# Kernel tuning notes

Hardware: AMD Instinct MI355X
Metric: run time of the kernel (lower is better)

## Reference

```python
import jax, jax.numpy as jnp
import numpy as np

THRESHOLD = 1.0   # spiking threshold (also used for reset detection)
BETA = 0.95       # reservoir membrane decay
N = 2048          # reservoir_size


def _heaviside(x):
    # snntorch Heaviside: (x > 0).float()
    return (x > 0).astype(x.dtype)


def setup_inputs() -> dict:
    key = jax.random.key(0)
    k1, k2, k3 = jax.random.split(key, 3)
    B, T = 32, 500
    x = jax.random.normal(k1, (B, T, 1), dtype=jnp.float32)
    # recurrent connectivity matrix loaded from .npy in the original; random here
    W = jax.random.normal(k2, (N, N), dtype=jnp.float32) / jnp.sqrt(jnp.float32(N))
    # nn.Linear default bias init: U(-1/sqrt(N), 1/sqrt(N))
    bound = 1.0 / np.sqrt(N)
    b = jax.random.uniform(k3, (N,), dtype=jnp.float32, minval=-bound, maxval=bound)
    return {"x": x, "W": W, "b": b}


def reference(x, W, b):
    """RLeaky reservoir with reset_mechanism='zero', reset_delay=True.
    Per step (snntorch RLeaky semantics):
      reset   = heaviside(mem_prev - threshold)            (detached)
      base    = beta*mem_prev + input + W @ spk_prev + b
      mem_new = base - reset*base                          ('zero' reset)
      spk_new = heaviside(mem_new - threshold)
    Input current = scalar x_t broadcast across all N neurons.
    """
    B = x.shape[0]
    Wt = W.T  # (N, N), spk @ W.T == Linear(spk)

    def step(carry, x_t):
        spk, mem = carry  # each (B, N)
        reset = _heaviside(mem - THRESHOLD)
        base = BETA * mem + x_t + spk @ Wt + b  # x_t: (B,1) broadcasts over N
        mem_new = base * (1.0 - reset)
        spk_new = _heaviside(mem_new - THRESHOLD)
        return (spk_new, mem_new), (spk_new, mem_new)

    init = (jnp.zeros((B, N), x.dtype), jnp.zeros((B, N), x.dtype))
    xs = jnp.swapaxes(x, 0, 1)  # (T, B, 1)
    _, (spk_rec, mem_rec) = jax.lax.scan(step, init, xs)
    avg_firing_rate = spk_rec.mean()
    return avg_firing_rate, spk_rec, mem_rec
```

## Files before the change

### kernel.cpp

```cpp
#include <hip/hip_runtime.h>

#define NN 2048
#define NB 32
#define NT 500
#define WGS 1024
#define NWG 256


__global__ void init_kernel(const float* __restrict__ x,
                            unsigned int* __restrict__ bitsG,
                            float* __restrict__ mem_ws,
                            float* __restrict__ xT,
                            int* __restrict__ wgcnt) {
    int g = blockIdx.x * blockDim.x + threadIdx.x;
    if (g < 2 * NN) bitsG[g] = 0u;
    if (g < NN * NB) mem_ws[g] = 0.0f;
    if (g < NT * NB) xT[g] = x[(size_t)(g & 31) * NT + (g >> 5)];
    if (g < NWG) wgcnt[g] = 0;
}

__launch_bounds__(WGS, 4)
__global__ void step_kernel(const float* __restrict__ W,
                            const float* __restrict__ bias,
                            float* __restrict__ out,
                            unsigned int* __restrict__ bitsG,
                            float* __restrict__ mem_ws,
                            const float* __restrict__ xT,
                            int* __restrict__ wgcnt,
                            int step)
{
    __shared__ unsigned int lbits[NN];
    __shared__ float lpart[8][8][32];
    __shared__ float lout[2][NB][9];
    __shared__ int   lcnt[4];

    const int wg = blockIdx.x;
    const int t  = threadIdx.x;
    const int i0 = wg * 8;
    const int cur = step & 1;

    ((uint2*)lbits)[t] = ((const uint2*)(bitsG + (size_t)cur * NN))[t];

    const int rh = t >> 8;
    const int jh = (t >> 5) & 7;
    const int b  = t & 31;

    float mem = 0.0f, xv = 0.0f, biasv = 0.0f;
    if (t < 256) {
        const int cil = t >> 5, cb = t & 31;
        mem   = mem_ws[(size_t)(i0 + cil) * NB + cb];
        xv    = xT[step * NB + cb];
        biasv = bias[i0 + cil];
    }

    const float4* __restrict__ wr0 = (const float4*)(W + (size_t)(i0 + 2 * rh    ) * NN) + jh * 64;
    const float4* __restrict__ wr1 = (const float4*)(W + (size_t)(i0 + 2 * rh + 1) * NN) + jh * 64;

    __syncthreads();

    float c0 = 0.0f, c1 = 0.0f;
    const uint4* bp = ((const uint4*)lbits) + jh * 64;
    #pragma unroll 4
    for (int jj = 0; jj < 64; ++jj) {
        const float4 w0 = wr0[jj];
        const float4 w1 = wr1[jj];
        const uint4  bu = bp[jj];
        float s;
        s = (float)((bu.x >> b) & 1u); c0 = fmaf(w0.x, s, c0); c1 = fmaf(w1.x, s, c1);
        s = (float)((bu.y >> b) & 1u); c0 = fmaf(w0.y, s, c0); c1 = fmaf(w1.y, s, c1);
        s = (float)((bu.z >> b) & 1u); c0 = fmaf(w0.z, s, c0); c1 = fmaf(w1.z, s, c1);
        s = (float)((bu.w >> b) & 1u); c0 = fmaf(w0.w, s, c0); c1 = fmaf(w1.w, s, c1);
    }
    lpart[jh][2 * rh    ][b] = c0;
    lpart[jh][2 * rh + 1][b] = c1;
    __syncthreads();

    if (t < 256) {
        const int cil = t >> 5;
        const int cb  = t & 31;

        float d = lpart[0][cil][cb];
        #pragma unroll
        for (int k = 1; k < 8; ++k) d += lpart[k][cil][cb];

        float sp = (float)((lbits[i0 + cil] >> cb) & 1u);

        float base = 0.95f * mem + xv + d + biasv;
        float nm   = base * (1.0f - sp);
        float ns   = (nm > 1.0f) ? 1.0f : 0.0f;

        mem_ws[(size_t)(i0 + cil) * NB + cb] = nm;

        unsigned long long bal = __ballot(ns > 0.5f);
        unsigned int* bw = bitsG + (size_t)(1 - cur) * NN;
        const int l  = t & 63;
        const int w2 = t >> 6;
        if (l == 0)  bw[i0 + 2 * w2]     = (unsigned int)(bal & 0xFFFFFFFFull);
        if (l == 32) bw[i0 + 2 * w2 + 1] = (unsigned int)(bal >> 32);
        if (l == 0)  lcnt[w2] = __popcll(bal);

        lout[0][cb][cil] = ns;
        lout[1][cb][cil] = nm;
    }
    __syncthreads();

    if (t == 0) wgcnt[wg] += lcnt[0] + lcnt[1] + lcnt[2] + lcnt[3];

    if (t < 512) {
        float* spk_rec = out + 1;
        float* mem_rec = out + 1 + (size_t)NT * NB * NN;
        const int arr = t >> 8;
        const int r2  = t & 255;
        const int bb  = r2 >> 3;
        const int il  = r2 & 7;
        size_t o = ((size_t)step * NB + bb) * (size_t)NN + i0 + il;
        if (arr == 0) __builtin_nontemporal_store(lout[0][bb][il], &spk_rec[o]);
        else          __builtin_nontemporal_store(lout[1][bb][il], &mem_rec[o]);
    }
}

__global__ void final_kernel(float* __restrict__ out, const int* __restrict__ wgcnt) {
    long long s = 0;
    for (int k = 0; k < NWG; ++k) s += wgcnt[k];
    out[0] = (float)((double)s / (double)((long long)NT * NB * NN));
}

extern "C" void kernel_launch(void* const* d_in, const int* in_sizes, int n_in,
                              void* d_out, int out_size, void* d_ws, size_t ws_size,
                              hipStream_t stream) {
    const float* x    = (const float*)d_in[0];
    const float* W    = (const float*)d_in[1];
    const float* bias = (const float*)d_in[2];
    float* out = (float*)d_out;

    unsigned int* bitsG  = (unsigned int*)d_ws;
    float*        mem_ws = (float*)((char*)d_ws + 16384);
    float*        xT     = (float*)((char*)d_ws + 278528);
    int*          wgcnt  = (int*)((char*)d_ws + 344064);

    init_kernel<<<dim3(256), dim3(256), 0, stream>>>(x, bitsG, mem_ws, xT, wgcnt);
    for (int step = 0; step < NT; ++step) {
        step_kernel<<<dim3(NWG), dim3(WGS), 0, stream>>>(W, bias, out, bitsG,
                                                         mem_ws, xT, wgcnt, step);
    }
    final_kernel<<<dim3(1), dim3(1), 0, stream>>>(out, wgcnt);
}
```

Baseline: 9.404 ms.

## Fuse time loop into persistent cooperative kernel with tagged spike-bit flags

Replaces the 500 per-step kernel launches with one cooperative persistent kernel that loops over all time steps. Membrane state stays in registers instead of global memory. Workgroups sync through per-word step tags packed into 64-bit spike-bit entries, polled with relaxed agent-scope atomics, rather than kernel boundaries. This removes launch overhead and the global round trip for membrane state, at the cost of relying on relaxed-ordering spin-polling across all 256 co-resident workgroups.

```diff
diff --git a/kernel.cpp b/kernel.cpp
--- a/kernel.cpp
+++ b/kernel.cpp
@@ -1,4 +1,7 @@
 #include <hip/hip_runtime.h>
+#include <hip/hip_cooperative_groups.h>
+
+namespace cg = cooperative_groups;
 
 #define NN 2048
 #define NB 32
@@ -7,122 +10,158 @@
 #define NWG 256
 
 
-__global__ void init_kernel(const float* __restrict__ x,
-                            unsigned int* __restrict__ bitsG,
-                            float* __restrict__ mem_ws,
-                            float* __restrict__ xT,
-                            int* __restrict__ wgcnt) {
-    int g = blockIdx.x * blockDim.x + threadIdx.x;
-    if (g < 2 * NN) bitsG[g] = 0u;
-    if (g < NN * NB) mem_ws[g] = 0.0f;
-    if (g < NT * NB) xT[g] = x[(size_t)(g & 31) * NT + (g >> 5)];
-    if (g < NWG) wgcnt[g] = 0;
-}
+__launch_bounds__(WGS, 4)
+__global__ void reservoir_kernel(const float* __restrict__ x,
+                                 const float* __restrict__ W,
+                                 const float* __restrict__ bias,
+                                 float* __restrict__ out,
+                                 void* __restrict__ wsv)
+{
+    cg::grid_group grid = cg::this_grid();
 
-__launch_bounds__(WGS, 4)
-__global__ void step_kernel(const float* __restrict__ W,
-                            const float* __restrict__ bias,
-                            float* __restrict__ out,
-                            unsigned int* __restrict__ bitsG,
-                            float* __restrict__ mem_ws,
-                            const float* __restrict__ xT,
-                            int* __restrict__ wgcnt,
-                            int step)
-{
     __shared__ unsigned int lbits[NN];
     __shared__ float lpart[8][8][32];
     __shared__ float lout[2][NB][9];
     __shared__ int   lcnt[4];
 
+    unsigned long long* bitsG2 = (unsigned long long*)wsv;
+    float* xT    = (float*)((char*)wsv + 32768);
+    int*   wgpart = (int*)((char*)wsv + 98304);
+
     const int wg = blockIdx.x;
     const int t  = threadIdx.x;
     const int i0 = wg * 8;
-    const int cur = step & 1;
 
-    ((uint2*)lbits)[t] = ((const uint2*)(bitsG + (size_t)cur * NN))[t];
+    if (t < 8) {
+        __hip_atomic_store(&bitsG2[i0 + t], 0ull,
+                           __ATOMIC_RELAXED, __HIP_MEMORY_SCOPE_AGENT);
+        __hip_atomic_store(&bitsG2[NN + i0 + t], 0xFFFFFFFF00000000ull,
+                           __ATOMIC_RELAXED, __HIP_MEMORY_SCOPE_AGENT);
+    }
+    for (int g = wg * WGS + t; g < NT * NB; g += NWG * WGS)
+        xT[g] = x[(size_t)(g & 31) * NT + (g >> 5)];
 
     const int rh = t >> 8;
     const int jh = (t >> 5) & 7;
     const int b  = t & 31;
 
-    float mem = 0.0f, xv = 0.0f, biasv = 0.0f;
-    if (t < 256) {
-        const int cil = t >> 5, cb = t & 31;
-        mem   = mem_ws[(size_t)(i0 + cil) * NB + cb];
-        xv    = xT[step * NB + cb];
-        biasv = bias[i0 + cil];
-    }
-
     const float4* __restrict__ wr0 = (const float4*)(W + (size_t)(i0 + 2 * rh    ) * NN) + jh * 64;
     const float4* __restrict__ wr1 = (const float4*)(W + (size_t)(i0 + 2 * rh + 1) * NN) + jh * 64;
 
+    const int cil = t >> 5;
+    const int cb  = t & 31;
+    const float biasv = (t < 256) ? bias[i0 + cil] : 0.0f;
+    float mem = 0.0f;
+    int   cnt = 0;
+
+    float* spk_rec = out + 1;
+    float* mem_rec = out + 1 + (size_t)NT * NB * NN;
+
+    grid.sync();
+
+    for (int step = 0; step < NT; ++step) {
+        const int cur = step & 1;
+        const unsigned int tag = (unsigned int)step;
+        const unsigned long long* src = bitsG2 + (size_t)cur * NN;
+
+        {
+            unsigned long long v;
+            for (;;) {
+                v = __hip_atomic_load(&src[t], __ATOMIC_RELAXED,
+                                      __HIP_MEMORY_SCOPE_AGENT);
+                if ((unsigned int)(v >> 32) == tag) break;
+                __builtin_amdgcn_s_sleep(1);
+            }
+            lbits[t] = (unsigned int)v;
+            for (;;) {
+                v = __hip_atomic_load(&src[t + 1024], __ATOMIC_RELAXED,
+                                      __HIP_MEMORY_SCOPE_AGENT);
+                if ((unsigned int)(v >> 32) == tag) break;
+                __builtin_amdgcn_s_sleep(1);
+            }
+            lbits[t + 1024] = (unsigned int)v;
+        }
+        const float xv = (t < 256) ? xT[step * NB + cb] : 0.0f;
+        __syncthreads();
+
+        float c0 = 0.0f, c1 = 0.0f;
+        const uint4* bp = ((const uint4*)lbits) + jh * 64;
+        #pragma unroll 4
+        for (int jj = 0; jj < 64; ++jj) {
+            const float4 w0 = wr0[jj];
+            const float4 w1 = wr1[jj];
+            const uint4  bu = bp[jj];
+            float s;
+            s = (float)((bu.x >> b) & 1u); c0 = fmaf(w0.x, s, c0); c1 = fmaf(w1.x, s, c1);
+            s = (float)((bu.y >> b) & 1u); c0 = fmaf(w0.y, s, c0); c1 = fmaf(w1.y, s, c1);
+            s = (float)((bu.z >> b) & 1u); c0 = fmaf(w0.z, s, c0); c1 = fmaf(w1.z, s, c1);
+            s = (float)((bu.w >> b) & 1u); c0 = fmaf(w0.w, s, c0); c1 = fmaf(w1.w, s, c1);
+        }
+        lpart[jh][2 * rh    ][b] = c0;
+        lpart[jh][2 * rh + 1][b] = c1;
+        __syncthreads();
+
+        if (t < 256) {
+            float d = lpart[0][cil][cb];
+            #pragma unroll
+            for (int k = 1; k < 8; ++k) d += lpart[k][cil][cb];
+
+            const float sp = (float)((lbits[i0 + cil] >> cb) & 1u);
+
+            float base = 0.95f * mem + xv + d + biasv;
+            float nm   = base * (1.0f - sp);
+            float ns   = (nm > 1.0f) ? 1.0f : 0.0f;
+            mem = nm;
+            cnt += (int)ns;
+
+            unsigned long long bal = __ballot(ns > 0.5f);
+            unsigned long long* dst = bitsG2 + (size_t)(1 - cur) * NN;
+            const unsigned long long tg = ((unsigned long long)(step + 1)) << 32;
+            const int l  = t & 63;
+            const int w2 = t >> 6;
+            if (l == 0)
+                __hip_atomic_store(&dst[i0 + 2 * w2],
+                                   tg | (unsigned int)(bal & 0xFFFFFFFFull),
+                                   __ATOMIC_RELAXED, __HIP_MEMORY_SCOPE_AGENT);
+            if (l == 32)
+                __hip_atomic_store(&dst[i0 + 2 * w2 + 1],
+                                   tg | (unsigned int)(bal >> 32),
+                                   __ATOMIC_RELAXED, __HIP_MEMORY_SCOPE_AGENT);
+            if (l == 0) lcnt[w2] = __popcll(bal);
+
+            lout[0][cb][cil] = ns;
+            lout[1][cb][cil] = nm;
+        }
+        __syncthreads();
+
+        if (t < 512) {
+            const int arr = t >> 8;
+            const int r2  = t & 255;
+            const int bb  = r2 >> 3;
+            const int il  = r2 & 7;
+            size_t o = ((size_t)step * NB + bb) * (size_t)NN + i0 + il;
+            if (arr == 0) __builtin_nontemporal_store(lout[0][bb][il], &spk_rec[o]);
+            else          __builtin_nontemporal_store(lout[1][bb][il], &mem_rec[o]);
+        }
+    }
+
+    #pragma unroll
+    for (int d2 = 1; d2 < 64; d2 <<= 1) cnt += __shfl_xor(cnt, d2, 64);
+    if ((t & 63) == 0 && t < 256) lcnt[t >> 6] = cnt;
     __syncthreads();
-
-    float c0 = 0.0f, c1 = 0.0f;
-    const uint4* bp = ((const uint4*)lbits) + jh * 64;
-    #pragma unroll 4
-    for (int jj = 0; jj < 64; ++jj) {
-        const float4 w0 = wr0[jj];
-        const float4 w1 = wr1[jj];
-        const uint4  bu = bp[jj];
-        float s;
-        s = (float)((bu.x >> b) & 1u); c0 = fmaf(w0.x, s, c0); c1 = fmaf(w1.x, s, c1);
-        s = (float)((bu.y >> b) & 1u); c0 = fmaf(w0.y, s, c0); c1 = fmaf(w1.y, s, c1);
-        s = (float)((bu.z >> b) & 1u); c0 = fmaf(w0.z, s, c0); c1 = fmaf(w1.z, s, c1);
-        s = (float)((bu.w >> b) & 1u); c0 = fmaf(w0.w, s, c0); c1 = fmaf(w1.w, s, c1);
+    if (t == 0) wgpart[wg] = lcnt[0] + lcnt[1] + lcnt[2] + lcnt[3];
+    grid.sync();
+    if (wg == 0) {
+        int ps = (t < NWG) ? wgpart[t] : 0;
+        #pragma unroll
+        for (int d2 = 1; d2 < 64; d2 <<= 1) ps += __shfl_xor(ps, d2, 64);
+        if ((t & 63) == 0 && t < 256) lcnt[t >> 6] = ps;
+        __syncthreads();
+        if (t == 0) {
+            long long s2 = (long long)lcnt[0] + lcnt[1] + lcnt[2] + lcnt[3];
+            out[0] = (float)((double)s2 / (double)((long long)NT * NB * NN));
+        }
     }
-    lpart[jh][2 * rh    ][b] = c0;
-    lpart[jh][2 * rh + 1][b] = c1;
-    __syncthreads();
-
-    if (t < 256) {
-        const int cil = t >> 5;
-        const int cb  = t & 31;
-
-        float d = lpart[0][cil][cb];
-        #pragma unroll
-        for (int k = 1; k < 8; ++k) d += lpart[k][cil][cb];
-
-        float sp = (float)((lbits[i0 + cil] >> cb) & 1u);
-
-        float base = 0.95f * mem + xv + d + biasv;
-        float nm   = base * (1.0f - sp);
-        float ns   = (nm > 1.0f) ? 1.0f : 0.0f;
-
-        mem_ws[(size_t)(i0 + cil) * NB + cb] = nm;
-
-        unsigned long long bal = __ballot(ns > 0.5f);
-        unsigned int* bw = bitsG + (size_t)(1 - cur) * NN;
-        const int l  = t & 63;
-        const int w2 = t >> 6;
-        if (l == 0)  bw[i0 + 2 * w2]     = (unsigned int)(bal & 0xFFFFFFFFull);
-        if (l == 32) bw[i0 + 2 * w2 + 1] = (unsigned int)(bal >> 32);
-        if (l == 0)  lcnt[w2] = __popcll(bal);
-
-        lout[0][cb][cil] = ns;
-        lout[1][cb][cil] = nm;
-    }
-    __syncthreads();
-
-    if (t == 0) wgcnt[wg] += lcnt[0] + lcnt[1] + lcnt[2] + lcnt[3];
-
-    if (t < 512) {
-        float* spk_rec = out + 1;
-        float* mem_rec = out + 1 + (size_t)NT * NB * NN;
-        const int arr = t >> 8;
-        const int r2  = t & 255;
-        const int bb  = r2 >> 3;
-        const int il  = r2 & 7;
-        size_t o = ((size_t)step * NB + bb) * (size_t)NN + i0 + il;
-        if (arr == 0) __builtin_nontemporal_store(lout[0][bb][il], &spk_rec[o]);
-        else          __builtin_nontemporal_store(lout[1][bb][il], &mem_rec[o]);
-    }
-}
-
-__global__ void final_kernel(float* __restrict__ out, const int* __restrict__ wgcnt) {
-    long long s = 0;
-    for (int k = 0; k < NWG; ++k) s += wgcnt[k];
-    out[0] = (float)((double)s / (double)((long long)NT * NB * NN));
 }
 
 extern "C" void kernel_launch(void* const* d_in, const int* in_sizes, int n_in,
@@ -132,16 +171,9 @@
     const float* W    = (const float*)d_in[1];
     const float* bias = (const float*)d_in[2];
     float* out = (float*)d_out;
+    void*  ws  = d_ws;
 
-    unsigned int* bitsG  = (unsigned int*)d_ws;
-    float*        mem_ws = (float*)((char*)d_ws + 16384);
-    float*        xT     = (float*)((char*)d_ws + 278528);
-    int*          wgcnt  = (int*)((char*)d_ws + 344064);
-
-    init_kernel<<<dim3(256), dim3(256), 0, stream>>>(x, bitsG, mem_ws, xT, wgcnt);
-    for (int step = 0; step < NT; ++step) {
-        step_kernel<<<dim3(NWG), dim3(WGS), 0, stream>>>(W, bias, out, bitsG,
-                                                         mem_ws, xT, wgcnt, step);
-    }
-    final_kernel<<<dim3(1), dim3(1), 0, stream>>>(out, wgcnt);
+    void* args[] = { (void*)&x, (void*)&W, (void*)&bias, (void*)&out, (void*)&ws };
+    hipLaunchCooperativeKernel((const void*)reservoir_kernel,
+                               dim3(NWG), dim3(WGS), args, 0, stream);
 }
```

Result: slower. 10.52 ms (+11.8%).
